# Optimization experiments

Measured on AMD Instinct MI355X. Metric: run time of the kernel, lower is better.

Reference implementation:

```python
import jax, jax.numpy as jnp
import numpy as np
from jax import lax


def fps(xyz, npoints):
    """Furthest point sampling. xyz: [B,N,3] -> indices [B,npoints] (int32).
    Matches the standard PointNet++ CUDA kernel: first index is 0, then
    iteratively pick the point furthest from the selected set."""
    B, N, _ = xyz.shape
    first = jnp.zeros((B,), jnp.int32)
    d0 = jnp.sum((xyz - xyz[:, :1]) ** 2, axis=-1)  # [B,N] dist^2 to point 0

    def body(dists, _):
        idx = jnp.argmax(dists, axis=-1).astype(jnp.int32)  # [B]
        p = jnp.take_along_axis(xyz, idx[:, None, None].astype(jnp.int32), axis=1)  # [B,1,3]
        d = jnp.sum((xyz - p) ** 2, axis=-1)  # [B,N]
        return jnp.minimum(dists, d), idx

    _, idxs = lax.scan(body, d0, None, length=npoints - 1)  # [npoints-1, B]
    return jnp.concatenate([first[None, :], idxs], axis=0).T  # [B, npoints]


def pointwise_mlp(x, w1, b1, w2, b2):
    # shared per-point MLP (stand-in for PointNet2SemSegSSGShape encoder)
    h = jax.nn.relu(jnp.einsum('bnc,cf->bnf', x, w1) + b1)
    return jnp.einsum('bnf,fg->bng', h, w2) + b2


def _level(points, npoints, w1, b1, w2, b2, repeat):
    # downSample: FPS on xyz (first 3 channels), gather full feature rows
    idx = fps(lax.stop_gradient(points[:, :, :3]), npoints)  # [B,npoints]
    down = jnp.take_along_axis(points, idx[:, :, None], axis=1)  # [B,npoints,C]
    inp = jnp.concatenate([down, down], axis=-1) if repeat else down
    feat = pointwise_mlp(inp, w1, b1, w2, b2)  # [B,npoints,feat_dim]
    # concat xyz with feat channels 3: (matches original cat + transpose)
    return jnp.concatenate([down[:, :, :3], feat[:, :, 3:]], axis=-1)


def setup_inputs() -> dict:
    key = jax.random.key(0)
    ks = jax.random.split(key, 17)
    B, N = 8, 8192
    scene_points = jax.random.normal(ks[0], (B, N, 3), jnp.float32)
    # encoder channel plan: (in_ch, feat_dim) per level
    plan = [(6, 16), (16, 32), (32, 64), (64, 128)]
    out = {'scene_points': scene_points}
    k = 1
    for li, (cin, f) in enumerate(plan, start=1):
        s1 = 1.0 / np.sqrt(cin)
        s2 = 1.0 / np.sqrt(f)
        out[f'w1_{li}'] = jax.random.normal(ks[k], (cin, f), jnp.float32) * s1; k += 1
        out[f'b1_{li}'] = jnp.zeros((f,), jnp.float32)
        out[f'w2_{li}'] = jax.random.normal(ks[k], (f, f), jnp.float32) * s2; k += 1
        out[f'b2_{li}'] = jnp.zeros((f,), jnp.float32)
    return out


def reference(scene_points,
              w1_1, b1_1, w2_1, b2_1,
              w1_2, b1_2, w2_2, b2_2,
              w1_3, b1_3, w2_3, b2_3,
              w1_4, b1_4, w2_4, b2_4):
    B, N, _ = scene_points.shape
    f1 = _level(scene_points, N // 2, w1_1, b1_1, w2_1, b2_1, repeat=True)
    f2 = _level(f1, N // 4, w1_2, b1_2, w2_2, b2_2, repeat=False)
    f3 = _level(f2, N // 8, w1_3, b1_3, w2_3, b2_3, repeat=False)
    f4 = _level(f3, N // 16, w1_4, b1_4, w2_4, b2_4, repeat=False)
    return (f1, f2, f3, f4)
```

## Files before the change

### kernel.cpp

```cpp
#include <hip/hip_runtime.h>

typedef float f32x2 __attribute__((ext_vector_type(2)));

__device__ __forceinline__ f32x2 pk_add(f32x2 a, f32x2 b) {
    f32x2 d; asm("v_pk_add_f32 %0, %1, %2" : "=v"(d) : "v"(a), "v"(b)); return d;
}
__device__ __forceinline__ f32x2 pk_mul(f32x2 a, f32x2 b) {
    f32x2 d; asm("v_pk_mul_f32 %0, %1, %2" : "=v"(d) : "v"(a), "v"(b)); return d;
}
__device__ __forceinline__ f32x2 pk_fma(f32x2 a, f32x2 b, f32x2 c) {
    f32x2 d; asm("v_pk_fma_f32 %0, %1, %2, %3" : "=v"(d) : "v"(a), "v"(b), "v"(c)); return d;
}

__device__ __forceinline__ double dist2d(float x, float y, float z,
                                         double px, double py, double pz) {
    double dx = __dsub_rn((double)x, px);
    double dy = __dsub_rn((double)y, py);
    double dz = __dsub_rn((double)z, pz);
    double a  = __dmul_rn(dx, dx);
    double b  = __dmul_rn(dy, dy);
    double c  = __dmul_rn(dz, dz);
    return __dadd_rn(__dadd_rn(a, b), c);
}

template <int CTRL>
__device__ __forceinline__ double dpp_f64_keep(double v) {
    long long b = __double_as_longlong(v);
    int lo = (int)(b & 0xFFFFFFFFLL);
    int hi = (int)(((unsigned long long)b) >> 32);
    int lo2 = __builtin_amdgcn_update_dpp(lo, lo, CTRL, 0xF, 0xF, false);
    int hi2 = __builtin_amdgcn_update_dpp(hi, hi, CTRL, 0xF, 0xF, false);
    return __longlong_as_double(((long long)(unsigned)hi2 << 32) | (unsigned)lo2);
}

__device__ __forceinline__ double wave_max_f64(double v) {
    v = fmax(v, dpp_f64_keep<0x111>(v));
    v = fmax(v, dpp_f64_keep<0x112>(v));
    v = fmax(v, dpp_f64_keep<0x114>(v));
    v = fmax(v, dpp_f64_keep<0x118>(v));
    v = fmax(v, dpp_f64_keep<0x142>(v));
    v = fmax(v, dpp_f64_keep<0x143>(v));
    return v;
}

__device__ __forceinline__ double readlane_f64(double v, int l) {
    long long b = __double_as_longlong(v);
    int lo = __builtin_amdgcn_readlane((int)(b & 0xFFFFFFFFLL), l);
    int hi = __builtin_amdgcn_readlane((int)(((unsigned long long)b) >> 32), l);
    return __longlong_as_double(((long long)(unsigned)hi << 32) | (unsigned)lo);
}

__device__ __forceinline__ float readlane_f32(float v, int l) {
    return __int_as_float(__builtin_amdgcn_readlane(__float_as_int(v), l));
}

template <int PPT, int NT>
__global__ __launch_bounds__(NT, 4) void fps_kernel(
    const float* __restrict__ pts,
    int stride, int npoints,
    int* __restrict__ idx_out)
{
    constexpr int NWAVES = NT / 64;
    constexpr int N_IN   = PPT * NT;
    constexpr int NPAIR  = PPT / 2;

    const int batch = blockIdx.x;
    const int tid   = threadIdx.x;
    const int lane  = tid & 63;
    const int wv    = tid >> 6;

    const float* base = pts + (size_t)batch * N_IN * stride;
    int* iout = idx_out + (size_t)batch * npoints;

    __shared__ double s_m[2][NWAVES];
    __shared__ int    s_i[2][NWAVES];
    __shared__ float4 s_c[2][NWAVES];
    __shared__ int    s_hist[4096];

    f32x2  pcx[NPAIR], pcy[NPAIR], pcz[NPAIR];
    double md[PPT];
    float  th[PPT];

#pragma unroll
    for (int k = 0; k < NPAIR; ++k) {
        int p0 = (2 * k) * NT + tid;
        int p1 = (2 * k + 1) * NT + tid;
        const float* r0 = base + (size_t)p0 * stride;
        const float* r1 = base + (size_t)p1 * stride;
        pcx[k] = f32x2{r0[0], r1[0]};
        pcy[k] = f32x2{r0[1], r1[1]};
        pcz[k] = f32x2{r0[2], r1[2]};
    }

    float q0x = base[0], q0y = base[1], q0z = base[2];
    if (tid == 0) s_hist[0] = 0;

    double bv = -1.0;
    int    bi = 0x7FFFFFFF;
    float  bx = 0.f, by = 0.f, bz = 0.f;
#pragma unroll
    for (int j = 0; j < PPT; ++j) {
        float x = pcx[j / 2][j & 1], y = pcy[j / 2][j & 1], z = pcz[j / 2][j & 1];
        md[j] = dist2d(x, y, z, (double)q0x, (double)q0y, (double)q0z);
        th[j] = __fmul_rn((float)md[j], 1.000004f);
        if (md[j] > bv) { bv = md[j]; bi = j * NT + tid; bx = x; by = y; bz = z; }
    }

    for (int i = 1; i < npoints; ++i) {
        const int par = i & 1;

        double wmax = readlane_f64(wave_max_f64(bv), 63);
        unsigned long long cm = __ballot(bv == wmax);
        int wl;
        if (__popcll(cm) == 1) {
            wl = __ffsll(cm) - 1;
        } else {
            int mi = 0x7FFFFFFF, ml = 0;
            unsigned long long t2 = cm;
            while (t2) {
                int l  = __ffsll(t2) - 1;
                int ci = __builtin_amdgcn_readlane(bi, l);
                if (ci < mi) { mi = ci; ml = l; }
                t2 &= t2 - 1;
            }
            wl = ml;
        }
        if (lane == 0) {
            int   wi = __builtin_amdgcn_readlane(bi, wl);
            float wx = readlane_f32(bx, wl);
            float wy = readlane_f32(by, wl);
            float wz = readlane_f32(bz, wl);
            s_m[par][wv] = wmax;
            s_i[par][wv] = wi;
            s_c[par][wv] = make_float4(wx, wy, wz, 0.0f);
        }
        __syncthreads();

        double pm   = s_m[par][lane & (NWAVES - 1)];
        int    pidx = s_i[par][lane & (NWAVES - 1)];
        double v2 = (lane < NWAVES) ? pm : -1.0;
        v2 = fmax(v2, dpp_f64_keep<0x111>(v2));
        v2 = fmax(v2, dpp_f64_keep<0x112>(v2));
        if (NWAVES >= 8)  v2 = fmax(v2, dpp_f64_keep<0x114>(v2));
        if (NWAVES >= 16) v2 = fmax(v2, dpp_f64_keep<0x118>(v2));
        double gmax = readlane_f64(v2, NWAVES - 1);
        unsigned long long c2 = __ballot((lane < NWAVES) && (pm == gmax));
        int wl2;
        if (__popcll(c2) == 1) {
            wl2 = __ffsll(c2) - 1;
        } else {
            int mi = 0x7FFFFFFF, ml = 0;
            unsigned long long t2 = c2;
            while (t2) {
                int l  = __ffsll(t2) - 1;
                int ci = __builtin_amdgcn_readlane(pidx, l);
                if (ci < mi) { mi = ci; ml = l; }
                t2 &= t2 - 1;
            }
            wl2 = ml;
        }
        int best = __builtin_amdgcn_readlane(pidx, wl2);
        if (tid == 0) s_hist[i] = best;

        float4 qc = s_c[par][wl2];
        const float qx = qc.x, qy = qc.y, qz = qc.z;
        const double qx64 = (double)qx, qy64 = (double)qy, qz64 = (double)qz;

        const f32x2 nqx = {-qx, -qx}, nqy = {-qy, -qy}, nqz = {-qz, -qz};
        int fmask = 0;
#pragma unroll
        for (int k = 0; k < NPAIR; ++k) {
            f32x2 dx = pk_add(pcx[k], nqx);
            f32x2 dy = pk_add(pcy[k], nqy);
            f32x2 dz = pk_add(pcz[k], nqz);
            f32x2 d  = pk_fma(dx, dx, pk_fma(dy, dy, pk_mul(dz, dz)));
            fmask |= (__any(d.x < th[2 * k])     ? (1 << (2 * k))     : 0);
            fmask |= (__any(d.y < th[2 * k + 1]) ? (1 << (2 * k + 1)) : 0);
        }

        if (fmask) {
#pragma unroll
            for (int j = 0; j < PPT; ++j) {
                if (fmask & (1 << j)) {
                    float x = pcx[j / 2][j & 1], y = pcy[j / 2][j & 1], z = pcz[j / 2][j & 1];
                    double d = dist2d(x, y, z, qx64, qy64, qz64);
                    md[j] = fmin(md[j], d);
                    th[j] = __fmul_rn((float)md[j], 1.000004f);
                }
            }
            bv = -1.0; bi = 0x7FFFFFFF;
#pragma unroll
            for (int j = 0; j < PPT; ++j) {
                if (md[j] > bv) {
                    bv = md[j]; bi = j * NT + tid;
                    bx = pcx[j / 2][j & 1]; by = pcy[j / 2][j & 1]; bz = pcz[j / 2][j & 1];
                }
            }
        }
    }

    __syncthreads();
    for (int i = tid; i < npoints; i += NT) iout[i] = s_hist[i];
}

template <int CIN, int F, bool REPEAT, bool IDENT>
__global__ __launch_bounds__(256) void mlp_kernel(
    const float* __restrict__ pts, int stride, int n_in,
    const int* __restrict__ idx,
    const float* __restrict__ w1, const float* __restrict__ b1,
    const float* __restrict__ w2, const float* __restrict__ b2,
    float* __restrict__ out, int np)
{
    constexpr int P    = 256 / F;
    constexpr int CINS = REPEAT ? (CIN / 2) : CIN;
    constexpr int LOGF = (F == 16) ? 4 : (F == 32) ? 5 : (F == 64) ? 6 : 7;

    __shared__ float xs[P][CINS];
    __shared__ float h[P][F];

    const int tid = threadIdx.x;
    const int pl  = tid >> LOGF;
    const int c   = tid & (F - 1);
    const int b   = blockIdx.y;
    const int pid = blockIdx.x * P + pl;

    const int id = IDENT ? pid : idx[(size_t)b * np + pid];
    const float* row = pts + ((size_t)b * n_in + id) * stride;

    if (c < CINS) xs[pl][c] = row[c];
    __syncthreads();

    float acc = b1[c];
#pragma unroll
    for (int k = 0; k < CIN; ++k) {
        const int xk = REPEAT ? (k % 3) : k;
        acc = fmaf(xs[pl][xk], w1[k * F + c], acc);
    }
    h[pl][c] = fmaxf(acc, 0.0f);
    __syncthreads();

    float acc2 = b2[c];
#pragma unroll
    for (int f = 0; f < F; ++f)
        acc2 = fmaf(h[pl][f], w2[f * F + c], acc2);

    float res = (c < 3) ? xs[pl][c] : acc2;
    out[((size_t)b * np + pid) * (size_t)F + c] = res;
}

extern "C" void kernel_launch(void* const* d_in, const int* in_sizes, int n_in_cnt,
                              void* d_out, int out_size, void* d_ws, size_t ws_size,
                              hipStream_t stream) {
    const float* scene = (const float*)d_in[0];
    const float* w1_1 = (const float*)d_in[1];
    const float* b1_1 = (const float*)d_in[2];
    const float* w2_1 = (const float*)d_in[3];
    const float* b2_1 = (const float*)d_in[4];
    const float* w1_2 = (const float*)d_in[5];
    const float* b1_2 = (const float*)d_in[6];
    const float* w2_2 = (const float*)d_in[7];
    const float* b2_2 = (const float*)d_in[8];
    const float* w1_3 = (const float*)d_in[9];
    const float* b1_3 = (const float*)d_in[10];
    const float* w2_3 = (const float*)d_in[11];
    const float* b2_3 = (const float*)d_in[12];
    const float* w1_4 = (const float*)d_in[13];
    const float* b1_4 = (const float*)d_in[14];
    const float* w2_4 = (const float*)d_in[15];
    const float* b2_4 = (const float*)d_in[16];

    float* out  = (float*)d_out;
    float* out1 = out;
    float* out2 = out + 524288;
    float* out3 = out + 1048576;
    float* out4 = out + 1572864;

    int* idx1 = (int*)d_ws;

    const int B = 8;

    fps_kernel<8, 1024><<<B, 1024, 0, stream>>>(scene, 3, 4096, idx1);
    mlp_kernel<6, 16, true, false><<<dim3(256, B), 256, 0, stream>>>(
        scene, 3, 8192, idx1, w1_1, b1_1, w2_1, b2_1, out1, 4096);

    mlp_kernel<16, 32, false, true><<<dim3(256, B), 256, 0, stream>>>(
        out1, 16, 4096, nullptr, w1_2, b1_2, w2_2, b2_2, out2, 2048);

    mlp_kernel<32, 64, false, true><<<dim3(256, B), 256, 0, stream>>>(
        out2, 32, 2048, nullptr, w1_3, b1_3, w2_3, b2_3, out3, 1024);

    mlp_kernel<64, 128, false, true><<<dim3(256, B), 256, 0, stream>>>(
        out3, 64, 1024, nullptr, w1_4, b1_4, w2_4, b2_4, out4, 512);
}
```

Measured before the change: 6.056 ms.

## Cache per-wave winners and reduce on high 32 bits of the double

Replaces the 64-bit double wave max with a 32-bit unsigned max on the high word of the nonnegative distance, breaking ties on the low word and the point index. Each wave's winner is cached and republished to shared memory only when a wave's local best actually shrinks, so the wave reduction is skipped on iterations where no lane's best changed. The query coordinates are read with readlane from registers loaded once, instead of a second indexed shared-memory load. This adds tie-break loops and bookkeeping state, and correctness relies on the bit ordering of positive doubles and on the new tie-break logic.

```diff
diff --git a/kernel.cpp b/kernel.cpp
--- a/kernel.cpp
+++ b/kernel.cpp
@@ -24,30 +24,18 @@
 }
 
 template <int CTRL>
-__device__ __forceinline__ double dpp_f64_keep(double v) {
-    long long b = __double_as_longlong(v);
-    int lo = (int)(b & 0xFFFFFFFFLL);
-    int hi = (int)(((unsigned long long)b) >> 32);
-    int lo2 = __builtin_amdgcn_update_dpp(lo, lo, CTRL, 0xF, 0xF, false);
-    int hi2 = __builtin_amdgcn_update_dpp(hi, hi, CTRL, 0xF, 0xF, false);
-    return __longlong_as_double(((long long)(unsigned)hi2 << 32) | (unsigned)lo2);
-}
-
-__device__ __forceinline__ double wave_max_f64(double v) {
-    v = fmax(v, dpp_f64_keep<0x111>(v));
-    v = fmax(v, dpp_f64_keep<0x112>(v));
-    v = fmax(v, dpp_f64_keep<0x114>(v));
-    v = fmax(v, dpp_f64_keep<0x118>(v));
-    v = fmax(v, dpp_f64_keep<0x142>(v));
-    v = fmax(v, dpp_f64_keep<0x143>(v));
+__device__ __forceinline__ unsigned dpp_u32_keep(unsigned v) {
+    return (unsigned)__builtin_amdgcn_update_dpp((int)v, (int)v, CTRL, 0xF, 0xF, false);
+}
+
+__device__ __forceinline__ unsigned wave_umax64(unsigned v) {
+    v = max(v, dpp_u32_keep<0x111>(v));
+    v = max(v, dpp_u32_keep<0x112>(v));
+    v = max(v, dpp_u32_keep<0x114>(v));
+    v = max(v, dpp_u32_keep<0x118>(v));
+    v = max(v, dpp_u32_keep<0x142>(v));
+    v = max(v, dpp_u32_keep<0x143>(v));
     return v;
-}
-
-__device__ __forceinline__ double readlane_f64(double v, int l) {
-    long long b = __double_as_longlong(v);
-    int lo = __builtin_amdgcn_readlane((int)(b & 0xFFFFFFFFLL), l);
-    int hi = __builtin_amdgcn_readlane((int)(((unsigned long long)b) >> 32), l);
-    return __longlong_as_double(((long long)(unsigned)hi << 32) | (unsigned)lo);
 }
 
 __device__ __forceinline__ float readlane_f32(float v, int l) {
@@ -63,6 +51,7 @@
     constexpr int NWAVES = NT / 64;
     constexpr int N_IN   = PPT * NT;
     constexpr int NPAIR  = PPT / 2;
+    constexpr int LOGNT  = (NT == 1024) ? 10 : (NT == 512) ? 9 : 8;
 
     const int batch = blockIdx.x;
     const int tid   = threadIdx.x;
@@ -72,8 +61,7 @@
     const float* base = pts + (size_t)batch * N_IN * stride;
     int* iout = idx_out + (size_t)batch * npoints;
 
-    __shared__ double s_m[2][NWAVES];
-    __shared__ int    s_i[2][NWAVES];
+    __shared__ uint2  s_pk[2][NWAVES];
     __shared__ float4 s_c[2][NWAVES];
     __shared__ int    s_hist[4096];
 
@@ -96,74 +84,100 @@
     if (tid == 0) s_hist[0] = 0;
 
     double bv = -1.0;
-    int    bi = 0x7FFFFFFF;
+    int    bj = 0;
     float  bx = 0.f, by = 0.f, bz = 0.f;
 #pragma unroll
     for (int j = 0; j < PPT; ++j) {
         float x = pcx[j / 2][j & 1], y = pcy[j / 2][j & 1], z = pcz[j / 2][j & 1];
         md[j] = dist2d(x, y, z, (double)q0x, (double)q0y, (double)q0z);
         th[j] = __fmul_rn((float)md[j], 1.000004f);
-        if (md[j] > bv) { bv = md[j]; bi = j * NT + tid; bx = x; by = y; bz = z; }
+        if (md[j] > bv) { bv = md[j]; bj = j; bx = x; by = y; bz = z; }
     }
 
-    for (int i = 1; i < npoints; ++i) {
-        const int par = i & 1;
-
-        double wmax = readlane_f64(wave_max_f64(bv), 63);
-        unsigned long long cm = __ballot(bv == wmax);
+    unsigned w_hi = 0, w_lo = 0;
+    int      w_i  = 0;
+    float    w_x = 0.f, w_y = 0.f, w_z = 0.f;
+    bool pub0 = false, pub1 = false;
+
+    auto reduce_winner = [&]() {
+        unsigned hi = (unsigned)__double2hiint(bv);
+        unsigned lo = (unsigned)__double2loint(bv);
+        int      bi = (bj << LOGNT) + tid;
+        unsigned maxhi = (unsigned)__builtin_amdgcn_readlane((int)wave_umax64(hi), 63);
+        unsigned long long cm = __ballot(hi == maxhi);
         int wl;
         if (__popcll(cm) == 1) {
             wl = __ffsll(cm) - 1;
         } else {
-            int mi = 0x7FFFFFFF, ml = 0;
+            unsigned bl = 0; int bidx = 0x7FFFFFFF; int ml = -1;
             unsigned long long t2 = cm;
             while (t2) {
-                int l  = __ffsll(t2) - 1;
-                int ci = __builtin_amdgcn_readlane(bi, l);
-                if (ci < mi) { mi = ci; ml = l; }
+                int l = __ffsll(t2) - 1;
+                unsigned lol = (unsigned)__builtin_amdgcn_readlane((int)lo, l);
+                int      il  = __builtin_amdgcn_readlane(bi, l);
+                if (ml < 0 || lol > bl || (lol == bl && il < bidx)) {
+                    bl = lol; bidx = il; ml = l;
+                }
                 t2 &= t2 - 1;
             }
             wl = ml;
         }
-        if (lane == 0) {
-            int   wi = __builtin_amdgcn_readlane(bi, wl);
-            float wx = readlane_f32(bx, wl);
-            float wy = readlane_f32(by, wl);
-            float wz = readlane_f32(bz, wl);
-            s_m[par][wv] = wmax;
-            s_i[par][wv] = wi;
-            s_c[par][wv] = make_float4(wx, wy, wz, 0.0f);
+        w_hi = maxhi;
+        w_lo = (unsigned)__builtin_amdgcn_readlane((int)lo, wl);
+        w_i  = __builtin_amdgcn_readlane(bi, wl);
+        w_x  = readlane_f32(bx, wl);
+        w_y  = readlane_f32(by, wl);
+        w_z  = readlane_f32(bz, wl);
+        pub0 = false; pub1 = false;
+    };
+    reduce_winner();
+
+    for (int i = 1; i < npoints; ++i) {
+        const int par = i & 1;
+
+        bool pub = par ? pub1 : pub0;
+        if (!pub) {
+            if (lane == 0) {
+                s_pk[par][wv] = make_uint2(w_hi, (unsigned)w_i);
+                s_c[par][wv]  = make_float4(w_x, w_y, w_z, __uint_as_float(w_lo));
+            }
+            if (par) pub1 = true; else pub0 = true;
         }
         __syncthreads();
 
-        double pm   = s_m[par][lane & (NWAVES - 1)];
-        int    pidx = s_i[par][lane & (NWAVES - 1)];
-        double v2 = (lane < NWAVES) ? pm : -1.0;
-        v2 = fmax(v2, dpp_f64_keep<0x111>(v2));
-        v2 = fmax(v2, dpp_f64_keep<0x112>(v2));
-        if (NWAVES >= 8)  v2 = fmax(v2, dpp_f64_keep<0x114>(v2));
-        if (NWAVES >= 16) v2 = fmax(v2, dpp_f64_keep<0x118>(v2));
-        double gmax = readlane_f64(v2, NWAVES - 1);
-        unsigned long long c2 = __ballot((lane < NWAVES) && (pm == gmax));
+        const int sl = lane & (NWAVES - 1);
+        uint2  pk = s_pk[par][sl];
+        float4 pc = s_c[par][sl];
+        unsigned v2 = (lane < NWAVES) ? pk.x : 0u;
+        v2 = max(v2, dpp_u32_keep<0x111>(v2));
+        v2 = max(v2, dpp_u32_keep<0x112>(v2));
+        if constexpr (NWAVES >= 8)  v2 = max(v2, dpp_u32_keep<0x114>(v2));
+        if constexpr (NWAVES >= 16) v2 = max(v2, dpp_u32_keep<0x118>(v2));
+        unsigned ghi = (unsigned)__builtin_amdgcn_readlane((int)v2, NWAVES - 1);
+        unsigned long long c2 = __ballot((lane < NWAVES) && (pk.x == ghi));
         int wl2;
         if (__popcll(c2) == 1) {
             wl2 = __ffsll(c2) - 1;
         } else {
-            int mi = 0x7FFFFFFF, ml = 0;
+            unsigned bl = 0; int bidx = 0x7FFFFFFF; int ml = -1;
             unsigned long long t2 = c2;
             while (t2) {
-                int l  = __ffsll(t2) - 1;
-                int ci = __builtin_amdgcn_readlane(pidx, l);
-                if (ci < mi) { mi = ci; ml = l; }
+                int l = __ffsll(t2) - 1;
+                unsigned lol = (unsigned)__builtin_amdgcn_readlane(__float_as_int(pc.w), l);
+                int      il  = __builtin_amdgcn_readlane((int)pk.y, l);
+                if (ml < 0 || lol > bl || (lol == bl && il < bidx)) {
+                    bl = lol; bidx = il; ml = l;
+                }
                 t2 &= t2 - 1;
             }
             wl2 = ml;
         }
-        int best = __builtin_amdgcn_readlane(pidx, wl2);
+        int best = __builtin_amdgcn_readlane((int)pk.y, wl2);
         if (tid == 0) s_hist[i] = best;
 
-        float4 qc = s_c[par][wl2];
-        const float qx = qc.x, qy = qc.y, qz = qc.z;
+        const float qx = readlane_f32(pc.x, wl2);
+        const float qy = readlane_f32(pc.y, wl2);
+        const float qz = readlane_f32(pc.z, wl2);
         const double qx64 = (double)qx, qy64 = (double)qy, qz64 = (double)qz;
 
         const f32x2 nqx = {-qx, -qx}, nqy = {-qy, -qy}, nqz = {-qz, -qz};
@@ -179,22 +193,28 @@
         }
 
         if (fmask) {
+            bool need = false;
 #pragma unroll
             for (int j = 0; j < PPT; ++j) {
                 if (fmask & (1 << j)) {
                     float x = pcx[j / 2][j & 1], y = pcy[j / 2][j & 1], z = pcz[j / 2][j & 1];
-                    double d = dist2d(x, y, z, qx64, qy64, qz64);
-                    md[j] = fmin(md[j], d);
+                    double d   = dist2d(x, y, z, qx64, qy64, qz64);
+                    double old = md[j];
+                    need = need | ((bj == j) & (d < old));
+                    md[j] = fmin(old, d);
                     th[j] = __fmul_rn((float)md[j], 1.000004f);
                 }
             }
-            bv = -1.0; bi = 0x7FFFFFFF;
-#pragma unroll
-            for (int j = 0; j < PPT; ++j) {
-                if (md[j] > bv) {
-                    bv = md[j]; bi = j * NT + tid;
-                    bx = pcx[j / 2][j & 1]; by = pcy[j / 2][j & 1]; bz = pcz[j / 2][j & 1];
+            if (__any(need)) {
+                bv = -1.0; bj = 0;
+#pragma unroll
+                for (int j = 0; j < PPT; ++j) {
+                    if (md[j] > bv) {
+                        bv = md[j]; bj = j;
+                        bx = pcx[j / 2][j & 1]; by = pcy[j / 2][j & 1]; bz = pcz[j / 2][j & 1];
+                    }
                 }
+                reduce_winner();
             }
         }
     }
```

Result: faster. 5.095 ms (-15.9%).
